# Performance work log

Measured on AMD Instinct MI355X. Metric: run time of the kernel, lower is better.

Reference implementation:

```python
import jax, jax.numpy as jnp
import numpy as np
from jax import lax

EPS = 1e-5  # BatchNorm eps; eval-mode BN with running_mean=0, running_var=1


def _bn(v, g, b):
    return v * (g / jnp.sqrt(1.0 + EPS)) + b


def setup_inputs() -> dict:
    key = jax.random.key(0)
    ks = jax.random.split(key, 8)
    B, I, O, H, W, E, K, r = 16, 128, 128, 128, 128, 16, 3, 8
    Ir, Or = I // r, O // r
    f = jax.random.normal
    return {
        "x": f(ks[0], (B, I, H, W), jnp.float32),
        "experts": f(ks[1], (E, O, I, K, K), jnp.float32) * 0.05,
        "rw1": f(ks[2], (Ir, I), jnp.float32) * 0.05,
        "rbn1_g": jnp.ones((Ir,), jnp.float32),
        "rbn1_b": jnp.zeros((Ir,), jnp.float32),
        "rw2": f(ks[3], (I, Ir), jnp.float32) * 0.05,
        "rbn2_g": jnp.ones((I,), jnp.float32),
        "rbn2_b": jnp.zeros((I,), jnp.float32),
        "rw3": f(ks[4], (E, I), jnp.float32) * 0.05,
        "rb3": jnp.zeros((E,), jnp.float32),
        "ca_w1": f(ks[5], (Or, O), jnp.float32) * 0.05,
        "ca_bn1_g": jnp.ones((Or,), jnp.float32),
        "ca_bn1_b": jnp.zeros((Or,), jnp.float32),
        "ca_w2": f(ks[6], (O, Or), jnp.float32) * 0.05,
        "ca_bn2_g": jnp.ones((O,), jnp.float32),
        "ca_bn2_b": jnp.zeros((O,), jnp.float32),
        "sa_w": f(ks[7], (1, 2, 7, 7), jnp.float32) * 0.05,
        "sa_bn_g": jnp.ones((1,), jnp.float32),
        "sa_bn_b": jnp.zeros((1,), jnp.float32),
    }


def reference(x, experts, rw1, rbn1_g, rbn1_b, rw2, rbn2_g, rbn2_b, rw3, rb3,
              ca_w1, ca_bn1_g, ca_bn1_b, ca_w2, ca_bn2_g, ca_bn2_b,
              sa_w, sa_bn_g, sa_bn_b):
    B, I, H, W = x.shape
    E, O, _, K, _ = experts.shape
    # --- routing: avgpool -> 1x1 conv (matmul) -> BN -> ReLU -> 1x1 -> BN -> sigmoid -> 1x1 -> softmax
    p = jnp.mean(x, axis=(2, 3))                                  # [B, I]
    h = jax.nn.relu(_bn(p @ rw1.T, rbn1_g, rbn1_b))               # [B, I/r]
    g = jax.nn.sigmoid(_bn(h @ rw2.T, rbn2_g, rbn2_b))            # [B, I]
    rweights = jax.nn.softmax(g @ rw3.T + rb3, axis=1)            # [B, E]
    # --- expert-weighted kernel generation as a single GEMM
    w = jnp.einsum('be,eoihw->boihw', rweights, experts)          # [B, O, I, K, K]
    # --- per-sample conv via grouped conv (groups = B), stride=1, padding=1
    out = lax.conv_general_dilated(
        x.reshape(1, B * I, H, W),
        w.reshape(B * O, I, K, K),
        window_strides=(1, 1), padding=((1, 1), (1, 1)),
        dimension_numbers=('NCHW', 'OIHW', 'NCHW'),
        feature_group_count=B,
    ).reshape(B, O, H, W)
    # --- SE channel attention
    cp = jnp.mean(out, axis=(2, 3))                               # [B, O]
    ch = jax.nn.relu(_bn(cp @ ca_w1.T, ca_bn1_g, ca_bn1_b))
    cw = jax.nn.sigmoid(_bn(ch @ ca_w2.T, ca_bn2_g, ca_bn2_b))    # [B, O]
    out = out * cw[:, :, None, None]
    # --- CBAM spatial attention
    sp = jnp.concatenate([jnp.mean(out, axis=1, keepdims=True),
                          jnp.max(out, axis=1, keepdims=True)], axis=1)  # [B,2,H,W]
    sw = lax.conv_general_dilated(sp, sa_w, (1, 1), ((3, 3), (3, 3)),
                                  dimension_numbers=('NCHW', 'OIHW', 'NCHW'))
    sw = jax.nn.sigmoid(_bn(sw, sa_bn_g.reshape(1, 1, 1, 1), sa_bn_b.reshape(1, 1, 1, 1)))
    out = out * sw
    # --- residual (in_channels == out_channels -> Identity)
    return out + x
```

## Files before the change

### kernel.cpp

```cpp
#include <hip/hip_runtime.h>

typedef unsigned short ushort_t;
typedef __attribute__((ext_vector_type(4))) float float4_t;
typedef __attribute__((ext_vector_type(8))) short short8_t;
typedef __attribute__((ext_vector_type(8))) unsigned short ushort8_t;

__device__ __forceinline__ ushort_t f2bf(float f) {
    unsigned u = __builtin_bit_cast(unsigned, f);
    u = (u + 0x7fffu + ((u >> 16) & 1u)) >> 16;
    return (ushort_t)u;
}

__device__ __forceinline__ void gld16(const void* g, void* l) {
    __builtin_amdgcn_global_load_lds(
        (const __attribute__((address_space(1))) unsigned int*)g,
        (__attribute__((address_space(3))) unsigned int*)l, 16, 0, 0);
}


__global__ __launch_bounds__(256) void init_kernel(float* __restrict__ p, float* __restrict__ cp,
                                                   float* __restrict__ sp, ushort_t* __restrict__ xn) {
    int t = blockIdx.x * 256 + threadIdx.x;
    if (t < 2048) { p[t] = 0.f; return; }
    if (t < 4096) { cp[t - 2048] = 0.f; return; }
    if (t < 4096 + 574592) { sp[t - 4096] = 0.f; return; }
    int e = t - (4096 + 574592);
    if (e < 1056768) {
        int b = e / 66048;
        int r = e % 66048;
        int pix = r >> 7, i = r & 127;
        int hp, wp;
        if (pix < 130)      { hp = 0;   wp = pix; }
        else if (pix < 260) { hp = 129; wp = pix - 130; }
        else { int q = pix - 260; hp = 1 + (q >> 1); wp = (q & 1) ? 129 : 0; }
        xn[((b * 130 + hp) * 130 + wp) * 128 + i] = 0;
    }
}

__global__ __launch_bounds__(256) void transpose_kernel(const float* __restrict__ x,
                                                        ushort_t* __restrict__ xn,
                                                        float* __restrict__ p) {
    __shared__ float tile[128][65];
    int blk = blockIdx.x;
    int wt = blk & 1, h = (blk >> 1) & 127, b = blk >> 8;
    int w0 = wt * 64;
    int tid = threadIdx.x;
    int wl = tid & 63, ig = tid >> 6;
    const float* src = x + ((long)(b * 128) * 128 + h) * 128 + w0 + wl;
    #pragma unroll
    for (int i = ig; i < 128; i += 4) tile[i][wl] = src[(long)i * 16384];
    __syncthreads();
    if (tid < 128) {
        float s = 0.f;
        #pragma unroll
        for (int w = 0; w < 64; ++w) s += tile[tid][w];
        atomicAdd(&p[b * 128 + tid], s * (1.0f / 16384.0f));
    }
    int l16 = tid & 15, wq = tid >> 4;
    #pragma unroll
    for (int pass = 0; pass < 4; ++pass) {
        int w = wq + pass * 16;
        ushort8_t v;
        #pragma unroll
        for (int j = 0; j < 8; ++j) v[j] = f2bf(tile[l16 * 8 + j][w]);
        *(ushort8_t*)&xn[((b * 130 + h + 1) * 130 + (w0 + w + 1)) * 128 + l16 * 8] = v;
    }
}

__global__ __launch_bounds__(256) void routing_kernel(const float* __restrict__ p,
        const float* __restrict__ rw1, const float* __restrict__ g1, const float* __restrict__ b1,
        const float* __restrict__ rw2, const float* __restrict__ g2, const float* __restrict__ b2,
        const float* __restrict__ rw3, const float* __restrict__ rb3, float* __restrict__ rwt) {
    __shared__ float sh[16][16];
    __shared__ float sg[16][128];
    __shared__ float sl[16][16];
    int tid = threadIdx.x;
    const float bns = rsqrtf(1.0f + 1e-5f);
    {   int b = tid >> 4, j = tid & 15;
        float s = 0.f;
        for (int i = 0; i < 128; ++i) s += p[b * 128 + i] * rw1[j * 128 + i];
        s = s * (g1[j] * bns) + b1[j];
        sh[b][j] = fmaxf(s, 0.f); }
    __syncthreads();
    for (int c = 0; c < 8; ++c) {
        int idx = tid + c * 256;
        int b = idx >> 7, j = idx & 127;
        float s = 0.f;
        for (int k = 0; k < 16; ++k) s += sh[b][k] * rw2[j * 16 + k];
        s = s * (g2[j] * bns) + b2[j];
        sg[b][j] = 1.0f / (1.0f + expf(-s));
    }
    __syncthreads();
    {   int b = tid >> 4, e = tid & 15;
        float s = rb3[e];
        for (int j = 0; j < 128; ++j) s += sg[b][j] * rw3[e * 128 + j];
        sl[b][e] = s; }
    __syncthreads();
    {   int b = tid >> 4, e = tid & 15;
        float m = -1e30f;
        for (int k = 0; k < 16; ++k) m = fmaxf(m, sl[b][k]);
        float num = expf(sl[b][e] - m), den = 0.f;
        for (int k = 0; k < 16; ++k) den += expf(sl[b][k] - m);
        rwt[b * 16 + e] = num / den; }
}

__global__ __launch_bounds__(256) void wgen_kernel(const float* __restrict__ experts,
                                                   const float* __restrict__ rwt,
                                                   ushort_t* __restrict__ w2) {
    int b = blockIdx.x >> 7, o = blockIdx.x & 127;
    int tid = threadIdx.x;
    int i = tid & 127, eh = tid >> 7;
    __shared__ float rw[16];
    __shared__ float part[9][128];
    if (tid < 16) rw[tid] = rwt[b * 16 + tid];
    __syncthreads();
    float acc[9] = {0, 0, 0, 0, 0, 0, 0, 0, 0};
    const float* ep = experts + (long)(eh * 8) * 147456 + (o * 128 + i) * 9;
    #pragma unroll
    for (int e = 0; e < 8; ++e) {
        float r = rw[eh * 8 + e];
        const float* q = ep + (long)e * 147456;
        #pragma unroll
        for (int d = 0; d < 9; ++d) acc[d] += r * q[d];
    }
    if (eh) {
        #pragma unroll
        for (int d = 0; d < 9; ++d) part[d][i] = acc[d];
    }
    __syncthreads();
    if (!eh) {
        #pragma unroll
        for (int d = 0; d < 9; ++d)
            w2[((b * 9 + d) << 14) + (o << 7) + i] = f2bf(acc[d] + part[d][i]);
    }
}

struct __align__(16) ConvSmem {
    union {
        struct { ushort_t X[16640]; ushort_t A[4][4096]; } t;
        float c[4224];
    };
};

__global__ __launch_bounds__(256, 2) void conv_kernel(const ushort_t* __restrict__ xn,
                                                      const ushort_t* __restrict__ w2,
                                                      float* __restrict__ out,
                                                      float* __restrict__ cp) {
    __shared__ ConvSmem sm;
    int bh = (blockIdx.x & 7) * 256 + (blockIdx.x >> 3);
    int b = bh >> 7, h = bh & 127;
    int tid = threadIdx.x;
    int lane = tid & 63, wave = tid >> 6;
    int wm = wave & 1, wn = wave >> 1;
    int q = lane >> 4, nl = lane & 15;

    float4_t acc[4][4];
    #pragma unroll
    for (int mi = 0; mi < 4; ++mi)
        #pragma unroll
        for (int ni = 0; ni < 4; ++ni) acc[mi][ni] = (float4_t){0.f, 0.f, 0.f, 0.f};

    const ushort_t* xbase = xn + (b * 130 + h) * 16640;
    const ushort_t* abase = w2 + (long)b * 147456;

    auto stageX = [&](int dy) {
        const ushort_t* xrow = xbase + dy * 16640;
        #pragma unroll
        for (int seg = wave; seg < 33; seg += 4) {
            if (seg < 32 || lane < 32) {
                int lofs = seg * 512 + lane * 8;
                int pp = lofs >> 7;
                int jb = (lofs & 127) >> 3;
                gld16(xrow + (pp << 7) + ((jb ^ (pp & 15)) << 3), &sm.t.X[seg * 512]);
            }
        }
    };
    auto stageA = [&](int c) {
        int dy = c / 12, rem = c % 12, dx = rem >> 2, ic = rem & 3;
        const ushort_t* ab = abase + (dy * 3 + dx) * 16384 + ic * 32;
        int buf = c & 3;
        int ol = lane >> 2;
        int jsrc = (lane & 3) ^ ((ol >> 1) & 3);
        #pragma unroll
        for (int inst = 0; inst < 2; ++inst) {
            int ob = wave * 32 + inst * 16;
            gld16(ab + (ob + ol) * 128 + (jsrc << 3), &sm.t.A[buf][ob * 32]);
        }
    };

    stageX(0);
    stageA(0); stageA(1); stageA(2);
    asm volatile("s_waitcnt vmcnt(0)" ::: "memory");
    __builtin_amdgcn_s_barrier();

    #pragma unroll
    for (int dy = 0; dy < 3; ++dy) {
        #pragma unroll
        for (int dx = 0; dx < 3; ++dx) {
            #pragma unroll
            for (int ic = 0; ic < 4; ++ic) {
                const int c = (dy * 3 + dx) * 4 + ic;
                if (c + 3 < 36) stageA(c + 3);
                const ushort_t* ap = &sm.t.A[c & 3][0];
                short8_t afr[4], bfr[4];
                #pragma unroll
                for (int mi = 0; mi < 4; ++mi) {
                    int o = wm * 64 + mi * 16 + nl;
                    afr[mi] = *(const short8_t*)&ap[(o << 5) + ((q ^ ((o >> 1) & 3)) << 3)];
                }
                #pragma unroll
                for (int ni = 0; ni < 4; ++ni) {
                    int pp = wn * 64 + ni * 16 + nl + dx;
                    int J = ic * 4 + q;
                    bfr[ni] = *(const short8_t*)&sm.t.X[(pp << 7) + ((J ^ (pp & 15)) << 3)];
                }
                __builtin_amdgcn_s_setprio(1);
                #pragma unroll
                for (int mi = 0; mi < 4; ++mi)
                    #pragma unroll
                    for (int ni = 0; ni < 4; ++ni)
                        acc[mi][ni] = __builtin_amdgcn_mfma_f32_16x16x32_bf16(
                            afr[mi], bfr[ni], acc[mi][ni], 0, 0, 0);
                __builtin_amdgcn_s_setprio(0);

                if (c == 11 || c == 23) {
                    __builtin_amdgcn_s_barrier();
                    stageX(dy + 1);
                    asm volatile("s_waitcnt vmcnt(0)" ::: "memory");
                    __builtin_amdgcn_s_barrier();
                } else if (c < 35) {
                    if (c != 0 && c != 1 && c != 12 && c != 13 && c != 24 && c != 25) {
                        if (c == 33)      asm volatile("s_waitcnt vmcnt(2)" ::: "memory");
                        else if (c == 34) asm volatile("s_waitcnt vmcnt(0)" ::: "memory");
                        else              asm volatile("s_waitcnt vmcnt(4)" ::: "memory");
                    }
                    __builtin_amdgcn_s_barrier();
                }
            }
        }
    }

    #pragma unroll
    for (int mi = 0; mi < 4; ++mi) {
        int o0 = wm * 64 + mi * 16 + q * 4;
        float rs[4] = {0.f, 0.f, 0.f, 0.f};
        #pragma unroll
        for (int ni = 0; ni < 4; ++ni) {
            float4_t v = acc[mi][ni];
            #pragma unroll
            for (int r = 0; r < 4; ++r) rs[r] += v[r];
        }
        #pragma unroll
        for (int r = 0; r < 4; ++r) {
            for (int msk = 1; msk < 16; msk <<= 1) rs[r] += __shfl_xor(rs[r], msk, 64);
            if (nl == 0) atomicAdd(&cp[(b << 7) + o0 + r], rs[r]);
        }
    }

    float* outb = out + (((long)(b << 7)) << 14) + (h << 7);
    #pragma unroll
    for (int os = 0; os < 4; ++os) {
        __syncthreads();
        if (wm == (os >> 1)) {
            #pragma unroll
            for (int mi2 = 0; mi2 < 2; ++mi2) {
                int mi = (os & 1) * 2 + mi2;
                #pragma unroll
                for (int ni = 0; ni < 4; ++ni) {
                    float4_t v = acc[mi][ni];
                    int orow = mi2 * 16 + q * 4;
                    int w = wn * 64 + ni * 16 + nl;
                    #pragma unroll
                    for (int rr = 0; rr < 4; ++rr) sm.c[(orow + rr) * 132 + w] = v[rr];
                }
            }
        }
        __syncthreads();
        int row = tid >> 3, j8 = tid & 7;
        float* og = outb + ((long)(os * 32 + row) << 14);
        #pragma unroll
        for (int k = 0; k < 4; ++k) {
            float4_t v = *(const float4_t*)&sm.c[row * 132 + j8 * 4 + k * 32];
            *(float4_t*)&og[j8 * 4 + k * 32] = v;
        }
    }
}

__global__ __launch_bounds__(256) void se_kernel(const float* __restrict__ cp,
        const float* __restrict__ w1, const float* __restrict__ g1, const float* __restrict__ b1,
        const float* __restrict__ w2, const float* __restrict__ g2, const float* __restrict__ b2,
        float* __restrict__ cw) {
    __shared__ float sc[16][128];
    __shared__ float sh[16][16];
    int tid = threadIdx.x;
    const float bns = rsqrtf(1.0f + 1e-5f);
    for (int c = 0; c < 8; ++c) {
        int idx = tid + c * 256;
        sc[idx >> 7][idx & 127] = cp[idx] * (1.0f / 16384.0f);
    }
    __syncthreads();
    {   int b = tid >> 4, j = tid & 15;
        float s = 0.f;
        for (int o = 0; o < 128; ++o) s += sc[b][o] * w1[j * 128 + o];
        s = s * (g1[j] * bns) + b1[j];
        sh[b][j] = fmaxf(s, 0.f); }
    __syncthreads();
    for (int c = 0; c < 8; ++c) {
        int idx = tid + c * 256;
        int b = idx >> 7, o = idx & 127;
        float s = 0.f;
        for (int k = 0; k < 16; ++k) s += sh[b][k] * w2[o * 16 + k];
        s = s * (g2[o] * bns) + b2[o];
        cw[idx] = 1.0f / (1.0f + expf(-s));
    }
}

__global__ __launch_bounds__(256) void stat_kernel(const float* __restrict__ out,
                                                   const float* __restrict__ cw,
                                                   float* __restrict__ sp) {
    int b = blockIdx.x >> 7, h = blockIdx.x & 127;
    int tid = threadIdx.x;
    int w = tid & 127, oh = tid >> 7;
    __shared__ float scw[128], ssum[128], smax[128];
    if (tid < 128) scw[tid] = cw[(b << 7) + tid];
    __syncthreads();
    const float* src = out + ((long)b << 21) + ((long)(oh * 64) << 14) + (h << 7) + w;
    float s = 0.f, m = -1e30f;
    #pragma unroll 8
    for (int o = 0; o < 64; ++o) {
        float v = src[(long)o << 14] * scw[oh * 64 + o];
        s += v;
        m = fmaxf(m, v);
    }
    if (oh) { ssum[w] = s; smax[w] = m; }
    __syncthreads();
    if (!oh) {
        s += ssum[w];
        m = fmaxf(m, smax[w]);
        float* d = sp + b * 2 * 17956;
        d[(h + 3) * 134 + (w + 3)] = s * (1.0f / 128.0f);
        d[17956 + (h + 3) * 134 + (w + 3)] = m;
    }
}

__global__ __launch_bounds__(256) void sattn_kernel(const float* __restrict__ sp,
        const float* __restrict__ k98, const float* __restrict__ g, const float* __restrict__ bb,
        const float* __restrict__ cw, const float* __restrict__ x, float* __restrict__ out) {
    int b = blockIdx.x >> 7, h = blockIdx.x & 127;
    int tid = threadIdx.x;
    __shared__ float ls[2][7][134];
    __shared__ float lk[98];
    __shared__ float sws[128];
    __shared__ float scw[128];
    const float* sb = sp + b * 2 * 17956;
    for (int idx = tid; idx < 2 * 7 * 134; idx += 256) {
        int c = idx / 938, rr = idx % 938;
        int ky = rr / 134, wp = rr % 134;
        ls[c][ky][wp] = sb[c * 17956 + (h + ky) * 134 + wp];
    }
    if (tid < 98) lk[tid] = k98[tid];
    if (tid >= 128) scw[tid - 128] = cw[(b << 7) + (tid - 128)];
    __syncthreads();
    if (tid < 128) {
        float s = 0.f;
        #pragma unroll
        for (int c = 0; c < 2; ++c)
            #pragma unroll
            for (int ky = 0; ky < 7; ++ky)
                #pragma unroll
                for (int kx = 0; kx < 7; ++kx)
                    s += ls[c][ky][tid + kx] * lk[c * 49 + ky * 7 + kx];
        s = s * (g[0] * rsqrtf(1.0f + 1e-5f)) + bb[0];
        sws[tid] = 1.0f / (1.0f + expf(-s));
    }
    __syncthreads();
    int w4 = tid & 31, og = tid >> 5;
    long base = (((long)b << 21) + (h << 7)) + (w4 << 2);
    float4_t sv = *(const float4_t*)&sws[w4 << 2];
    #pragma unroll
    for (int o = og; o < 128; o += 8) {
        long idx = base + ((long)o << 14);
        float4_t ov = *(const float4_t*)&out[idx];
        float4_t xv = *(const float4_t*)&x[idx];
        float4_t r = ov * scw[o] * sv + xv;
        *(float4_t*)&out[idx] = r;
    }
}

extern "C" void kernel_launch(void* const* d_in, const int* in_sizes, int n_in,
                              void* d_out, int out_size, void* d_ws, size_t ws_size,
                              hipStream_t stream) {
    const float* x       = (const float*)d_in[0];
    const float* experts = (const float*)d_in[1];
    const float* rw1     = (const float*)d_in[2];
    const float* rbn1_g  = (const float*)d_in[3];
    const float* rbn1_b  = (const float*)d_in[4];
    const float* rw2     = (const float*)d_in[5];
    const float* rbn2_g  = (const float*)d_in[6];
    const float* rbn2_b  = (const float*)d_in[7];
    const float* rw3     = (const float*)d_in[8];
    const float* rb3     = (const float*)d_in[9];
    const float* ca_w1   = (const float*)d_in[10];
    const float* ca_bn1g = (const float*)d_in[11];
    const float* ca_bn1b = (const float*)d_in[12];
    const float* ca_w2   = (const float*)d_in[13];
    const float* ca_bn2g = (const float*)d_in[14];
    const float* ca_bn2b = (const float*)d_in[15];
    const float* sa_w    = (const float*)d_in[16];
    const float* sa_g    = (const float*)d_in[17];
    const float* sa_b    = (const float*)d_in[18];
    float* out = (float*)d_out;
    char* ws = (char*)d_ws;

    ushort_t* xn  = (ushort_t*)(ws);
    ushort_t* w2  = (ushort_t*)(ws + 69222400);
    float*    p   = (float*)(ws + 73940992);
    float*    cp  = (float*)(ws + 73949184);
    float*    rwt = (float*)(ws + 73957376);
    float*    cw  = (float*)(ws + 73958400);
    float*    sp  = (float*)(ws + 73966592);

    hipLaunchKernelGGL(init_kernel, dim3(6389), dim3(256), 0, stream, p, cp, sp, xn);
    hipLaunchKernelGGL(transpose_kernel, dim3(4096), dim3(256), 0, stream, x, xn, p);
    hipLaunchKernelGGL(routing_kernel, dim3(1), dim3(256), 0, stream,
                       p, rw1, rbn1_g, rbn1_b, rw2, rbn2_g, rbn2_b, rw3, rb3, rwt);
    hipLaunchKernelGGL(wgen_kernel, dim3(2048), dim3(256), 0, stream, experts, rwt, w2);
    hipLaunchKernelGGL(conv_kernel, dim3(2048), dim3(256), 0, stream, xn, w2, out, cp);
    hipLaunchKernelGGL(se_kernel, dim3(1), dim3(256), 0, stream,
                       cp, ca_w1, ca_bn1g, ca_bn1b, ca_w2, ca_bn2g, ca_bn2b, cw);
    hipLaunchKernelGGL(stat_kernel, dim3(2048), dim3(256), 0, stream, out, cw, sp);
    hipLaunchKernelGGL(sattn_kernel, dim3(2048), dim3(256), 0, stream,
                       sp, sa_w, sa_g, sa_b, cw, x, out);
}
```

Measured before the change: 502.4 us.

## Double-buffer MFMA register fragments to prefetch next LDS chunk during compute

Restructures the 36-step conv main loop so the A and X fragments for step c+1 are read from LDS into a second register buffer while the MFMAs for step c run. The aim is to hide LDS read latency behind matrix-core work. The vmcnt waits are retuned to match, so each A stage is resident before its early fragment read. This roughly doubles the fragment registers, which may raise VGPR pressure and lower occupancy, and the three dy boundaries still serialize on barriers.

```diff
diff --git a/kernel.cpp b/kernel.cpp
--- a/kernel.cpp
+++ b/kernel.cpp
@@ -188,55 +188,58 @@
         }
     };
 
+    short8_t afr[2][4], bfr[2][4];
+    auto readFrag = [&](int cc) {
+        int pb = cc & 1;
+        int dx = (cc % 12) >> 2, ic = cc & 3;
+        const ushort_t* ap = &sm.t.A[cc & 3][0];
+        #pragma unroll
+        for (int mi = 0; mi < 4; ++mi) {
+            int o = wm * 64 + mi * 16 + nl;
+            afr[pb][mi] = *(const short8_t*)&ap[(o << 5) + ((q ^ ((o >> 1) & 3)) << 3)];
+        }
+        #pragma unroll
+        for (int ni = 0; ni < 4; ++ni) {
+            int pp = wn * 64 + ni * 16 + nl + dx;
+            int J = ic * 4 + q;
+            bfr[pb][ni] = *(const short8_t*)&sm.t.X[(pp << 7) + ((J ^ (pp & 15)) << 3)];
+        }
+    };
+    auto domfma = [&](int pb) {
+        __builtin_amdgcn_s_setprio(1);
+        #pragma unroll
+        for (int mi = 0; mi < 4; ++mi)
+            #pragma unroll
+            for (int ni = 0; ni < 4; ++ni)
+                acc[mi][ni] = __builtin_amdgcn_mfma_f32_16x16x32_bf16(
+                    afr[pb][mi], bfr[pb][ni], acc[pb ? mi : mi][ni], 0, 0, 0);
+        __builtin_amdgcn_s_setprio(0);
+    };
+
     stageX(0);
     stageA(0); stageA(1); stageA(2);
     asm volatile("s_waitcnt vmcnt(0)" ::: "memory");
     __builtin_amdgcn_s_barrier();
-
-    #pragma unroll
-    for (int dy = 0; dy < 3; ++dy) {
-        #pragma unroll
-        for (int dx = 0; dx < 3; ++dx) {
-            #pragma unroll
-            for (int ic = 0; ic < 4; ++ic) {
-                const int c = (dy * 3 + dx) * 4 + ic;
-                if (c + 3 < 36) stageA(c + 3);
-                const ushort_t* ap = &sm.t.A[c & 3][0];
-                short8_t afr[4], bfr[4];
-                #pragma unroll
-                for (int mi = 0; mi < 4; ++mi) {
-                    int o = wm * 64 + mi * 16 + nl;
-                    afr[mi] = *(const short8_t*)&ap[(o << 5) + ((q ^ ((o >> 1) & 3)) << 3)];
-                }
-                #pragma unroll
-                for (int ni = 0; ni < 4; ++ni) {
-                    int pp = wn * 64 + ni * 16 + nl + dx;
-                    int J = ic * 4 + q;
-                    bfr[ni] = *(const short8_t*)&sm.t.X[(pp << 7) + ((J ^ (pp & 15)) << 3)];
-                }
-                __builtin_amdgcn_s_setprio(1);
-                #pragma unroll
-                for (int mi = 0; mi < 4; ++mi)
-                    #pragma unroll
-                    for (int ni = 0; ni < 4; ++ni)
-                        acc[mi][ni] = __builtin_amdgcn_mfma_f32_16x16x32_bf16(
-                            afr[mi], bfr[ni], acc[mi][ni], 0, 0, 0);
-                __builtin_amdgcn_s_setprio(0);
-
-                if (c == 11 || c == 23) {
-                    __builtin_amdgcn_s_barrier();
-                    stageX(dy + 1);
-                    asm volatile("s_waitcnt vmcnt(0)" ::: "memory");
-                    __builtin_amdgcn_s_barrier();
-                } else if (c < 35) {
-                    if (c != 0 && c != 1 && c != 12 && c != 13 && c != 24 && c != 25) {
-                        if (c == 33)      asm volatile("s_waitcnt vmcnt(2)" ::: "memory");
-                        else if (c == 34) asm volatile("s_waitcnt vmcnt(0)" ::: "memory");
-                        else              asm volatile("s_waitcnt vmcnt(4)" ::: "memory");
-                    }
-                    __builtin_amdgcn_s_barrier();
-                }
-            }
+    readFrag(0);
+
+    #pragma unroll
+    for (int c = 0; c < 36; ++c) {
+        if (c + 3 < 36) stageA(c + 3);
+        const bool bnd = (c == 11 || c == 23);
+        if (!bnd && c + 1 < 36) readFrag(c + 1);
+        domfma(c & 1);
+        if (bnd) {
+            __builtin_amdgcn_s_barrier();
+            stageX(c == 11 ? 1 : 2);
+            asm volatile("s_waitcnt vmcnt(0)" ::: "memory");
+            __builtin_amdgcn_s_barrier();
+            readFrag(c + 1);
+        } else if (c < 35) {
+            if (c == 33)
+                asm volatile("s_waitcnt vmcnt(0)" ::: "memory");
+            else if (!(c == 0 || c == 12 || c == 24 || c == 34))
+                asm volatile("s_waitcnt vmcnt(2)" ::: "memory");
+            __builtin_amdgcn_s_barrier();
         }
     }
 
```

After: 489.8 us. -2.5%, faster.
